# Optimization experiments

Measured on AMD Instinct MI355X. Metric: run time of the kernel, lower is better.

The kernel has to match this reference:

```python
import jax, jax.numpy as jnp
import numpy as np
import math

B, S, D, H = 4, 2048, 1024, 16
DH = D // H  # head dim = 64


def setup_inputs() -> dict:
    key = jax.random.key(0)
    ks = jax.random.split(key, 6)
    x = jax.random.normal(ks[0], (B, S, D), dtype=jnp.float32)
    mask = jax.random.randint(ks[1], (B, 1, S, S), 0, 2, dtype=jnp.int32)
    # torch nn.Linear default init scale ~ 1/sqrt(fan_in); use small scale for stability
    w_qkv = jax.random.normal(ks[2], (D, 3 * D), dtype=jnp.float32) * (1.0 / math.sqrt(D))
    b_qkv = jax.random.normal(ks[3], (3 * D,), dtype=jnp.float32) * 0.01
    w_out = jax.random.normal(ks[4], (D, D), dtype=jnp.float32) * (1.0 / math.sqrt(D))
    b_out = jax.random.normal(ks[5], (D,), dtype=jnp.float32) * 0.01
    return {"x": x, "mask": mask, "w_qkv": w_qkv, "b_qkv": b_qkv, "w_out": w_out, "b_out": b_out}


def reference(x, mask, w_qkv, b_qkv, w_out, b_out):
    # Fused QKV projection: [B,S,3D]
    qkv = x @ w_qkv + b_qkv
    q, k, v = qkv[..., :D], qkv[..., D:2 * D], qkv[..., 2 * D:]
    # split heads -> [B,H,S,DH]
    def split(t):
        return t.reshape(B, S, H, DH).transpose(0, 2, 1, 3)
    q, k, v = split(q), split(k), split(v)
    # scores: [B,H,S,S]
    scores = jnp.einsum("bhqd,bhkd->bhqk", q, k) / jnp.sqrt(jnp.float32(DH))
    scores = jnp.where(mask == 0, jnp.float32(-1000.0), scores)
    attn = jax.nn.softmax(scores, axis=-1)
    ctx = jnp.einsum("bhqk,bhkd->bhqd", attn, v)  # [B,H,S,DH]
    ctx = ctx.transpose(0, 2, 1, 3).reshape(B, S, D)
    return ctx @ w_out + b_out
```

## Files before the change

kernel.cpp:

```cpp
#include <hip/hip_runtime.h>
#include <hip/hip_bf16.h>
#include <stdint.h>

#define B_  4
#define S_  2048
#define D_  1024
#define H_  16
#define DH_ 64
#define N3_ 3072

typedef __attribute__((ext_vector_type(8))) short  short8;
typedef __attribute__((ext_vector_type(8))) unsigned short ushort8;
typedef __attribute__((ext_vector_type(4))) float  float4v;

__device__ __forceinline__ float bf2f(unsigned short u) {
    union { unsigned int i; float f; } c; c.i = ((unsigned int)u) << 16; return c.f;
}
__device__ __forceinline__ unsigned short f2bf(float f) {
    union { float f; unsigned int i; } c; c.f = f;
    unsigned int x = c.i;
    return (unsigned short)((x + 0x7FFFu + ((x >> 16) & 1u)) >> 16);
}
__device__ __forceinline__ unsigned short f2bf_hu(float f) {
    union { float f; unsigned int i; } c; c.f = f;
    return (unsigned short)((c.i + 0x8000u) >> 16);
}

__device__ __forceinline__ void gll16(const void* g, void* l) {
    __builtin_amdgcn_global_load_lds(
        (const __attribute__((address_space(1))) unsigned int*)g,
        (__attribute__((address_space(3))) unsigned int*)l, 16, 0, 0);
}

__global__ __launch_bounds__(256) void convert_x(
    const float* __restrict__ in, unsigned short* __restrict__ out, int n8)
{
    int g = blockIdx.x * 256 + threadIdx.x;
    if (g >= n8) return;
    const float4* p = (const float4*)(in + (size_t)g * 8);
    float4 a = p[0], b = p[1];
    ushort8 o;
    o[0] = f2bf(a.x); o[1] = f2bf(a.y); o[2] = f2bf(a.z); o[3] = f2bf(a.w);
    o[4] = f2bf(b.x); o[5] = f2bf(b.y); o[6] = f2bf(b.z); o[7] = f2bf(b.w);
    *(ushort8*)(out + (size_t)g * 8) = o;
}

__global__ __launch_bounds__(256) void convert_wT(
    const float* __restrict__ w, unsigned short* __restrict__ wt, int K, int N)
{
    __shared__ float t[32][33];
    const int row = threadIdx.x >> 5;
    const int col = threadIdx.x & 31;
    const int n0 = blockIdx.x * 32;
    const int k0 = blockIdx.y * 32;
#pragma unroll
    for (int i = 0; i < 4; ++i)
        t[row + 8 * i][col] = w[(size_t)(k0 + row + 8 * i) * N + n0 + col];
    __syncthreads();
#pragma unroll
    for (int i = 0; i < 4; ++i)
        wt[(size_t)(n0 + row + 8 * i) * K + k0 + col] = f2bf(t[col][row + 8 * i]);
}

template <int MODE>
__global__ __launch_bounds__(256) void gemm_bt(
    const unsigned short* __restrict__ a, const unsigned short* __restrict__ bt,
    const float* __restrict__ bias,
    unsigned short* __restrict__ q, unsigned short* __restrict__ k,
    unsigned short* __restrict__ v, float* __restrict__ out,
    int K, int N)
{
    __shared__ unsigned short As[128][64];
    __shared__ unsigned short Bs[128][64];

    const int tid  = threadIdx.x;
    const int wave = tid >> 6;
    const int lane = tid & 63;
    const int col  = lane & 15;
    const int quad = lane >> 4;
    const int wm   = (wave & 1) * 64;
    const int wn   = (wave >> 1) * 64;

    const int m0 = blockIdx.y * 128;
    const int n0 = blockIdx.x * 128;

    const int srow0 = wave * 32 + (lane >> 3);
    const int scg   = (lane & 7) ^ (lane >> 3);

    float4v acc[4][4] = {};

    for (int kt = 0; kt < K; kt += 64) {
#pragma unroll
        for (int c = 0; c < 4; ++c) {
            int row = srow0 + c * 8;
            gll16(a  + (size_t)(m0 + row) * K + kt + scg * 8,
                  (char*)As + wave * 4096 + c * 1024);
            gll16(bt + (size_t)(n0 + row) * K + kt + scg * 8,
                  (char*)Bs + wave * 4096 + c * 1024);
        }
        __syncthreads();

#pragma unroll
        for (int ks = 0; ks < 64; ks += 32) {
            const int sa = (((ks >> 3) + quad) ^ (col & 7)) * 8;
            short8 af[4], bf[4];
#pragma unroll
            for (int mi = 0; mi < 4; ++mi)
                af[mi] = *(const short8*)&As[wm + mi * 16 + col][sa];
#pragma unroll
            for (int ni = 0; ni < 4; ++ni)
                bf[ni] = *(const short8*)&Bs[wn + ni * 16 + col][sa];
#pragma unroll
            for (int mi = 0; mi < 4; ++mi)
#pragma unroll
                for (int ni = 0; ni < 4; ++ni)
                    acc[mi][ni] = __builtin_amdgcn_mfma_f32_16x16x32_bf16(
                        af[mi], bf[ni], acc[mi][ni], 0, 0, 0);
        }
        __syncthreads();
    }

#pragma unroll
    for (int mi = 0; mi < 4; ++mi) {
#pragma unroll
        for (int ni = 0; ni < 4; ++ni) {
            int n = n0 + wn + ni * 16 + col;
            float bv = bias[n];
#pragma unroll
            for (int r = 0; r < 4; ++r) {
                int m = m0 + wm + mi * 16 + quad * 4 + r;
                float val = acc[mi][ni][r] + bv;
                if (MODE == 0) {
                    int which = n >> 10;
                    int h  = (n & 1023) >> 6;
                    int dh = n & 63;
                    int bb = m >> 11;
                    int s  = m & 2047;
                    size_t off;
                    if (which == 2)
                        off = (((size_t)bb * H_ + h) * DH_ + dh) * S_ + s;
                    else
                        off = (((size_t)bb * H_ + h) * S_ + s) * DH_ + dh;
                    unsigned short* dst = (which == 0) ? q : ((which == 1) ? k : v);
                    dst[off] = f2bf(val);
                } else {
                    out[(size_t)m * N + n] = val;
                }
            }
        }
    }
}

__global__ __launch_bounds__(256) void attn_mfma(
    const unsigned short* __restrict__ q, const unsigned short* __restrict__ k,
    const unsigned short* __restrict__ vT, const int* __restrict__ mask,
    unsigned short* __restrict__ ctx)
{
    __shared__ unsigned short Ks[2][64][64];
    __shared__ unsigned short Vt[2][64][64];
    __shared__ unsigned short Ps[4][16][64];

    const int tid  = threadIdx.x;
    const int wave = tid >> 6;
    const int lane = tid & 63;
    const int col  = lane & 15;
    const int quad = lane >> 4;

    const int h  = blockIdx.y;
    const int bb = blockIdx.z;
    const int q0 = blockIdx.x * 64 + wave * 16;
    const int kvbase = ((bb * H_ + h) * S_) * DH_;
    const int vtbase = ((bb * H_ + h) * DH_) * S_;

    const float SC = 0.18033688011112042f;
    const unsigned short* qrow = q + kvbase + (q0 + col) * DH_;
    ushort8 qr0 = *(const ushort8*)(qrow + quad * 8);
    ushort8 qr1 = *(const ushort8*)(qrow + 32 + quad * 8);
    short8 qa0, qa1;
#pragma unroll
    for (int j = 0; j < 8; ++j) {
        qa0[j] = (short)f2bf(bf2f(qr0[j]) * SC);
        qa1[j] = (short)f2bf(bf2f(qr1[j]) * SC);
    }
    const float MASKED = -1442.6951f;

    const int* mrow = mask + ((size_t)bb * S_ + q0 + col) * S_ + quad * 4;

    const int sw2   = wave & 1;
    const int srow0 = sw2 * 32 + (lane >> 3);
    const int scg   = (lane & 7) ^ (lane >> 3);
    const int sw0   = (quad ^ (col & 7)) * 8;
    const int sw1   = ((4 + quad) ^ (col & 7)) * 8;

    float4v oacc[4] = {};
    float rsum = 0.f;

    auto STAGE = [&](int buf, int kt) {
        const int key0 = kt * 64;
#pragma unroll
        for (int c = 0; c < 4; ++c) {
            int r = srow0 + c * 8;
            if (wave < 2)
                gll16(k + kvbase + (key0 + r) * DH_ + scg * 8,
                      (char*)Ks + buf * 8192 + sw2 * 4096 + c * 1024);
            else
                gll16(vT + vtbase + r * S_ + key0 + scg * 8,
                      (char*)Vt + buf * 8192 + sw2 * 4096 + c * 1024);
        }
    };

    auto LOADMASK = [&](int4 (&m)[4], int kt) {
        const int* p = mrow + kt * 64;
#pragma unroll
        for (int sub = 0; sub < 4; ++sub)
            m[sub] = *(const int4*)(p + sub * 16);
    };

    auto TILE = [&](int buf, const int4 (&mu)[4]) {
        float4v sc[4];
#pragma unroll
        for (int sub = 0; sub < 4; ++sub) {
            short8 a0 = *(const short8*)&Ks[buf][sub * 16 + col][sw0];
            short8 a1 = *(const short8*)&Ks[buf][sub * 16 + col][sw1];
            float4v acs = {};
            acs = __builtin_amdgcn_mfma_f32_16x16x32_bf16(a0, qa0, acs, 0, 0, 0);
            acs = __builtin_amdgcn_mfma_f32_16x16x32_bf16(a1, qa1, acs, 0, 0, 0);
            sc[sub] = acs;
        }
#pragma unroll
        for (int sub = 0; sub < 4; ++sub) {
            int mm[4] = { mu[sub].x, mu[sub].y, mu[sub].z, mu[sub].w };
            float p[4];
#pragma unroll
            for (int r = 0; r < 4; ++r) {
                float s = (mm[r] == 0) ? MASKED : sc[sub][r];
                p[r] = __builtin_amdgcn_exp2f(s);
                rsum += p[r];
            }
            unsigned int u0 = ((unsigned int)f2bf_hu(p[1]) << 16) | f2bf_hu(p[0]);
            unsigned int u1 = ((unsigned int)f2bf_hu(p[3]) << 16) | f2bf_hu(p[2]);
            int sg = (2 * sub + (quad >> 1)) ^ (col & 7);
            uint2 w; w.x = u0; w.y = u1;
            *(uint2*)((char*)&Ps[wave][0][0] + col * 128 + sg * 16 + (quad & 1) * 8) = w;
        }
        short8 pa0 = *(const short8*)&Ps[wave][col][sw0];
        short8 pa1 = *(const short8*)&Ps[wave][col][sw1];
#pragma unroll
        for (int n = 0; n < 4; ++n) {
            short8 vb0 = *(const short8*)&Vt[buf][n * 16 + col][sw0];
            short8 vb1 = *(const short8*)&Vt[buf][n * 16 + col][sw1];
            oacc[n] = __builtin_amdgcn_mfma_f32_16x16x32_bf16(pa0, vb0, oacc[n], 0, 0, 0);
            oacc[n] = __builtin_amdgcn_mfma_f32_16x16x32_bf16(pa1, vb1, oacc[n], 0, 0, 0);
        }
    };

    int4 mA[4], mB[4];
    LOADMASK(mA, 0);
    STAGE(0, 0);
#pragma unroll 1
    for (int kt2 = 0; kt2 < S_ / 128; ++kt2) {
        const int ke = kt2 * 2, ko = ke + 1;
        __syncthreads();
        LOADMASK(mB, ko);
        STAGE(1, ko);
        TILE(0, mA);
        __syncthreads();
        if (kt2 < S_ / 128 - 1) {
            LOADMASK(mA, ke + 2);
            STAGE(0, ke + 2);
        }
        TILE(1, mB);
    }

    float s = rsum;
    s += __shfl_xor(s, 16);
    s += __shfl_xor(s, 32);
    float invs = 1.0f / s;
    float inv4[4];
#pragma unroll
    for (int r = 0; r < 4; ++r)
        inv4[r] = __shfl(invs, quad * 20 + r);
#pragma unroll
    for (int n = 0; n < 4; ++n)
#pragma unroll
    for (int r = 0; r < 4; ++r) {
        size_t off = ((size_t)bb * S_ + (q0 + quad * 4 + r)) * D_
                   + h * DH_ + n * 16 + col;
        ctx[off] = f2bf(oacc[n][r] * inv4[r]);
    }
}

extern "C" void kernel_launch(void* const* d_in, const int* in_sizes, int n_in,
                              void* d_out, int out_size, void* d_ws, size_t ws_size,
                              hipStream_t stream)
{
    const float* x     = (const float*)d_in[0];
    const int*   mask  = (const int*)d_in[1];
    const float* w_qkv = (const float*)d_in[2];
    const float* b_qkv = (const float*)d_in[3];
    const float* w_out = (const float*)d_in[4];
    const float* b_out = (const float*)d_in[5];
    float* out = (float*)d_out;

    unsigned short* ws = (unsigned short*)d_ws;
    const size_t sz = (size_t)B_ * S_ * D_;
    unsigned short* q     = ws;
    unsigned short* kk    = ws + sz;
    unsigned short* v     = ws + 2 * sz;
    unsigned short* ctx   = ws + 3 * sz;
    unsigned short* xbf   = ws + 4 * sz;
    unsigned short* wqkvT = ws + 5 * sz;
    unsigned short* woutT = ws + 5 * sz + (size_t)N3_ * D_;

    convert_x<<<(int)(sz / (256 * 8)), 256, 0, stream>>>(x, xbf, (int)(sz / 8));
    convert_wT<<<dim3(N3_ / 32, D_ / 32), 256, 0, stream>>>(w_qkv, wqkvT, D_, N3_);
    convert_wT<<<dim3(D_ / 32, D_ / 32), 256, 0, stream>>>(w_out, woutT, D_, D_);

    gemm_bt<0><<<dim3(N3_ / 128, (B_ * S_) / 128), 256, 0, stream>>>(
        xbf, wqkvT, b_qkv, q, kk, v, nullptr, D_, N3_);

    attn_mfma<<<dim3(S_ / 64, H_, B_), 256, 0, stream>>>(q, kk, v, mask, ctx);

    gemm_bt<1><<<dim3(D_ / 128, (B_ * S_) / 128), 256, 0, stream>>>(
        ctx, woutT, b_out, nullptr, nullptr, nullptr, out, D_, D_);
}
```

Before: 421.9 us.

## Replace double-buffered K/V staging with single-buffer loop and packed bf16 convert

Removes the double-buffered K/V LDS staging and mask prefetch, so each 64-key tile is loaded, synchronized, and consumed in one plain loop. P conversion uses the hardware v_cvt_pk_bf16_f32 instruction instead of manual rounding. The P LDS swizzle becomes 8-byte granular, and the row-sum adds are regrouped. The change halves K/V shared memory, which may raise occupancy, but it loses the overlap of global loads with compute.

```diff
diff --git a/kernel.cpp b/kernel.cpp
--- a/kernel.cpp
+++ b/kernel.cpp
@@ -21,9 +21,10 @@
     unsigned int x = c.i;
     return (unsigned short)((x + 0x7FFFu + ((x >> 16) & 1u)) >> 16);
 }
-__device__ __forceinline__ unsigned short f2bf_hu(float f) {
-    union { float f; unsigned int i; } c; c.f = f;
-    return (unsigned short)((c.i + 0x8000u) >> 16);
+__device__ __forceinline__ unsigned int cvt_pk_bf16(float a, float b) {
+    unsigned int r;
+    asm("v_cvt_pk_bf16_f32 %0, %1, %2" : "=v"(r) : "v"(a), "v"(b));
+    return r;
 }
 
 __device__ __forceinline__ void gll16(const void* g, void* l) {
@@ -156,8 +157,8 @@
     const unsigned short* __restrict__ vT, const int* __restrict__ mask,
     unsigned short* __restrict__ ctx)
 {
-    __shared__ unsigned short Ks[2][64][64];
-    __shared__ unsigned short Vt[2][64][64];
+    __shared__ unsigned short Ks[64][64];
+    __shared__ unsigned short Vt[64][64];
     __shared__ unsigned short Ps[4][16][64];
 
     const int tid  = threadIdx.x;
@@ -192,41 +193,42 @@
     const int sw0   = (quad ^ (col & 7)) * 8;
     const int sw1   = ((4 + quad) ^ (col & 7)) * 8;
 
+    char* psW = (char*)Ps + wave * 2048;
+
     float4v oacc[4] = {};
     float rsum = 0.f;
 
-    auto STAGE = [&](int buf, int kt) {
+    for (int kt = 0; kt < S_ / 64; ++kt) {
         const int key0 = kt * 64;
+
+        int4 mu[4];
+#pragma unroll
+        for (int sub = 0; sub < 4; ++sub)
+            mu[sub] = *(const int4*)(mrow + key0 + sub * 16);
+
 #pragma unroll
         for (int c = 0; c < 4; ++c) {
             int r = srow0 + c * 8;
             if (wave < 2)
                 gll16(k + kvbase + (key0 + r) * DH_ + scg * 8,
-                      (char*)Ks + buf * 8192 + sw2 * 4096 + c * 1024);
+                      (char*)Ks + sw2 * 4096 + c * 1024);
             else
                 gll16(vT + vtbase + r * S_ + key0 + scg * 8,
-                      (char*)Vt + buf * 8192 + sw2 * 4096 + c * 1024);
-        }
-    };
-
-    auto LOADMASK = [&](int4 (&m)[4], int kt) {
-        const int* p = mrow + kt * 64;
-#pragma unroll
-        for (int sub = 0; sub < 4; ++sub)
-            m[sub] = *(const int4*)(p + sub * 16);
-    };
-
-    auto TILE = [&](int buf, const int4 (&mu)[4]) {
+                      (char*)Vt + sw2 * 4096 + c * 1024);
+        }
+        __syncthreads();
+
         float4v sc[4];
 #pragma unroll
         for (int sub = 0; sub < 4; ++sub) {
-            short8 a0 = *(const short8*)&Ks[buf][sub * 16 + col][sw0];
-            short8 a1 = *(const short8*)&Ks[buf][sub * 16 + col][sw1];
+            short8 a0 = *(const short8*)&Ks[sub * 16 + col][sw0];
+            short8 a1 = *(const short8*)&Ks[sub * 16 + col][sw1];
             float4v acs = {};
             acs = __builtin_amdgcn_mfma_f32_16x16x32_bf16(a0, qa0, acs, 0, 0, 0);
             acs = __builtin_amdgcn_mfma_f32_16x16x32_bf16(a1, qa1, acs, 0, 0, 0);
             sc[sub] = acs;
         }
+
 #pragma unroll
         for (int sub = 0; sub < 4; ++sub) {
             int mm[4] = { mu[sub].x, mu[sub].y, mu[sub].z, mu[sub].w };
@@ -235,41 +237,32 @@
             for (int r = 0; r < 4; ++r) {
                 float s = (mm[r] == 0) ? MASKED : sc[sub][r];
                 p[r] = __builtin_amdgcn_exp2f(s);
-                rsum += p[r];
             }
-            unsigned int u0 = ((unsigned int)f2bf_hu(p[1]) << 16) | f2bf_hu(p[0]);
-            unsigned int u1 = ((unsigned int)f2bf_hu(p[3]) << 16) | f2bf_hu(p[2]);
-            int sg = (2 * sub + (quad >> 1)) ^ (col & 7);
-            uint2 w; w.x = u0; w.y = u1;
-            *(uint2*)((char*)&Ps[wave][0][0] + col * 128 + sg * 16 + (quad & 1) * 8) = w;
-        }
-        short8 pa0 = *(const short8*)&Ps[wave][col][sw0];
-        short8 pa1 = *(const short8*)&Ps[wave][col][sw1];
+            rsum += (p[0] + p[1]) + (p[2] + p[3]);
+            uint2 w;
+            w.x = cvt_pk_bf16(p[0], p[1]);
+            w.y = cvt_pk_bf16(p[2], p[3]);
+            int t = ((sub << 2) + quad) ^ col;
+            *(uint2*)(psW + col * 128 + t * 8) = w;
+        }
+
+        uint2 l0 = *(const uint2*)(psW + col * 128 + (((quad << 1) + 0) ^ col) * 8);
+        uint2 l1 = *(const uint2*)(psW + col * 128 + (((quad << 1) + 1) ^ col) * 8);
+        uint2 l2 = *(const uint2*)(psW + col * 128 + (((quad << 1) + 8) ^ col) * 8);
+        uint2 l3 = *(const uint2*)(psW + col * 128 + (((quad << 1) + 9) ^ col) * 8);
+        union { uint4 u; short8 s8; } c0, c1;
+        c0.u.x = l0.x; c0.u.y = l0.y; c0.u.z = l1.x; c0.u.w = l1.y;
+        c1.u.x = l2.x; c1.u.y = l2.y; c1.u.z = l3.x; c1.u.w = l3.y;
+        short8 pa0 = c0.s8, pa1 = c1.s8;
+
 #pragma unroll
         for (int n = 0; n < 4; ++n) {
-            short8 vb0 = *(const short8*)&Vt[buf][n * 16 + col][sw0];
-            short8 vb1 = *(const short8*)&Vt[buf][n * 16 + col][sw1];
+            short8 vb0 = *(const short8*)&Vt[n * 16 + col][sw0];
+            short8 vb1 = *(const short8*)&Vt[n * 16 + col][sw1];
             oacc[n] = __builtin_amdgcn_mfma_f32_16x16x32_bf16(pa0, vb0, oacc[n], 0, 0, 0);
             oacc[n] = __builtin_amdgcn_mfma_f32_16x16x32_bf16(pa1, vb1, oacc[n], 0, 0, 0);
         }
-    };
-
-    int4 mA[4], mB[4];
-    LOADMASK(mA, 0);
-    STAGE(0, 0);
-#pragma unroll 1
-    for (int kt2 = 0; kt2 < S_ / 128; ++kt2) {
-        const int ke = kt2 * 2, ko = ke + 1;
         __syncthreads();
-        LOADMASK(mB, ko);
-        STAGE(1, ko);
-        TILE(0, mA);
-        __syncthreads();
-        if (kt2 < S_ / 128 - 1) {
-            LOADMASK(mA, ke + 2);
-            STAGE(0, ke + 2);
-        }
-        TILE(1, mB);
     }
 
     float s = rsum;
```

Result: no change. 422.2 us (+0.1%).
